# Kernel tuning notes

Hardware: AMD Instinct MI355X
Metric: run time of the kernel (lower is better)

The kernel has to match this reference:

```python
import jax, jax.numpy as jnp
import numpy as np

B, CIN, COUT, K, S, P = 16, 32, 64, 5, 2, 2
D, H, W = 16, 32, 32


def setup_inputs() -> dict:
    key = jax.random.key(0)
    k1, k2, k3 = jax.random.split(key, 3)
    x = jax.random.normal(k1, (B, CIN, D, H, W), dtype=jnp.float32)
    # PyTorch ConvTranspose3d weight layout: (in_channels, out_channels, kD, kH, kW)
    fan = CIN * K * K * K
    bound = 1.0 / np.sqrt(fan)
    weight = jax.random.uniform(k2, (CIN, COUT, K, K, K), dtype=jnp.float32, minval=-bound, maxval=bound)
    bias = jax.random.uniform(k3, (COUT,), dtype=jnp.float32, minval=-bound, maxval=bound)
    return {"x": x, "weight": weight, "bias": bias}


def _maxpool3d(y, k):
    # MaxPool3d with kernel=stride=k, no padding (PyTorch default stride=kernel)
    return jax.lax.reduce_window(y, -jnp.inf, jax.lax.max,
                                 (1, 1, k, k, k), (1, 1, k, k, k), 'VALID')


def reference(x, weight, bias):
    # ConvTranspose3d == conv with lhs_dilation=stride, padding k-1-p, flipped kernel,
    # with (in,out) kernel axes swapped to OIDHW.
    kernel = jnp.flip(weight, axis=(2, 3, 4)).transpose(1, 0, 2, 3, 4)  # (COUT, CIN, K, K, K)
    y = jax.lax.conv_general_dilated(
        x, kernel,
        window_strides=(1, 1, 1),
        padding=[(K - 1 - P, K - 1 - P)] * 3,
        lhs_dilation=(S, S, S),
        dimension_numbers=('NCDHW', 'OIDHW', 'NCDHW'))  # [B, COUT, 31, 63, 63]
    y = y + bias[None, :, None, None, None]
    y = _maxpool3d(y, 2)   # [B, COUT, 15, 31, 31]
    y = _maxpool3d(y, 3)   # [B, COUT, 5, 10, 10]
    return jnp.sum(y, axis=1, keepdims=True)  # [B, 1, 5, 10, 10]
```

## Files before the change

kernel.cpp:

```cpp
#include <hip/hip_runtime.h>


typedef __attribute__((ext_vector_type(8))) short short8;
typedef __attribute__((ext_vector_type(4))) float f32x4;

#define CIN 32
#define COUT 64

static __device__ __forceinline__ short f2bf(float f) {
  unsigned u = __float_as_uint(f);
  return (short)((u + 0x7fffu + ((u >> 16) & 1u)) >> 16);
}

__global__ __launch_bounds__(256) void reorder_w(const float* __restrict__ w,
                                                 short* __restrict__ wr) {
  const int t = blockIdx.x * 256 + threadIdx.x;
  const int l = t & 63, mt = (t >> 6) & 3, tap = t >> 8;
  const int cout = 16 * mt + (l & 15);
  const int kb = l >> 4;
  short8 v;
#pragma unroll
  for (int j = 0; j < 8; ++j)
    v[j] = f2bf(w[((8 * kb + j) * COUT + cout) * 125 + tap]);
  *(short8*)&wr[t * 8] = v;
}

#define E0 (0ULL | 1ULL<<6 | 2ULL<<12 | 27ULL<<18 | 52ULL<<24 | 5ULL<<30 | 6ULL<<36 | 7ULL<<42)
#define E1 (32ULL | 25ULL<<6 | 26ULL<<12 | 51ULL<<18 | 12ULL<<24 | 37ULL<<30 | 30ULL<<36 | 55ULL<<42)
#define O0 (56ULL | 57ULL<<6 | 50ULL<<12 | 11ULL<<18 | 36ULL<<24 | 61ULL<<30 | 62ULL<<36 | 31ULL<<42)
#define O1 (0ULL | 1ULL<<6 | 10ULL<<12 | 35ULL<<18 | 60ULL<<24 | 5ULL<<30 | 6ULL<<36 | 7ULL<<42)

__global__ __launch_bounds__(512) void convt_mfma_r11(
    const float* __restrict__ x, const short* __restrict__ wr,
    const float* __restrict__ bias, float* __restrict__ out) {
  __shared__ short xs[8 * 4 * 125 * 8];
  __shared__ float red[16];

  const int orig = blockIdx.x;
  const int bi = (orig & 7) * 125 + (orig >> 3);
  const int bg = bi / 500, r = bi % 500;
  const int od = r / 100, oh = (r / 10) % 10, ow = r % 10;
  const int tid = threadIdx.x;
  const int d0 = 3 * od - 1, h0 = 3 * oh - 1, w0 = 3 * ow - 1;
  const int xoff0 = d0 * 1024 + h0 * 32 + w0;

  for (int e = tid; e < 8 * 4 * 128; e += 512) {
    const int pos = e & 127;
    if (pos < 125) {
      const int kb = (e >> 7) & 3, bb = e >> 9;
      const int id = pos / 25, rem = pos - 25 * id;
      const int ih = rem / 5, iw = rem - 5 * ih;
      const bool ok = (d0 + id) >= 0 && (h0 + ih) >= 0 && (w0 + iw) >= 0;
      const float* xp =
          x + ((size_t)((bg * 8 + bb) * CIN + kb * 8) << 14) + xoff0 + id * 1024 + ih * 32 + iw;
      short8 v8;
#pragma unroll
      for (int j = 0; j < 8; ++j) v8[j] = f2bf(ok ? xp[j << 14] : 0.f);
      *(short8*)&xs[(bb * 500 + kb * 125 + pos) * 8] = v8;
    }
  }
  __syncthreads();

  const int lane = tid & 63, wv = tid >> 6;
  const int mhat = wv >> 2;
  const int bp = wv & 3;
  const int kb = lane >> 4, c = lane & 15;

  const int pos_e = (int)((c < 8 ? (E0 >> (6 * c)) : (E1 >> (6 * (c - 8)))) & 63ULL);
  const int pos_o = (int)((c < 8 ? (O0 >> (6 * c)) : (O1 >> (6 * (c - 8)))) & 63ULL);

  int baddr[4];
#pragma unroll
  for (int i = 0; i < 4; ++i) {
    const int bb = 2 * bp + (i >> 1);
    baddr[i] = (bb * 500 + kb * 125 + ((i & 1) ? pos_o : pos_e)) * 8;
  }

  float mreg[2][2][4];
#pragma unroll
  for (int mm = 0; mm < 2; ++mm)
#pragma unroll
    for (int bl = 0; bl < 2; ++bl)
#pragma unroll
      for (int q = 0; q < 4; ++q) mreg[mm][bl][q] = -__builtin_inff();

  const short* __restrict__ wbase = wr + (2 * mhat) * 512 + lane * 8;

#pragma unroll 1
  for (int p = 0; p < 8; ++p) {
    const int pd = p >> 2, ph = (p >> 1) & 1, pw = p & 1;
    f32x4 acc[2][4];
#pragma unroll
    for (int mm = 0; mm < 2; ++mm)
#pragma unroll
      for (int i = 0; i < 4; ++i) acc[mm][i] = (f32x4){0.f, 0.f, 0.f, 0.f};

#pragma unroll 1
    for (int td = 0; td <= 2 - pd; ++td)
      for (int th = 0; th <= 2 - ph; ++th)
        for (int tw = 0; tw <= 2 - pw; ++tw) {
          const int tap = (pd + 2 * td) * 25 + (ph + 2 * th) * 5 + (pw + 2 * tw);
          const int toff8 = ((2 - td) * 25 + (2 - th) * 5 + (2 - tw)) * 8;
          short8 af[2];
#pragma unroll
          for (int mm = 0; mm < 2; ++mm)
            af[mm] = *(const short8*)(wbase + tap * 2048 + mm * 512);
          short8 bfr[4];
#pragma unroll
          for (int i = 0; i < 4; ++i)
            bfr[i] = *(const short8*)&xs[baddr[i] + toff8];
#pragma unroll
          for (int mm = 0; mm < 2; ++mm)
#pragma unroll
            for (int i = 0; i < 4; ++i)
              acc[mm][i] = __builtin_amdgcn_mfma_f32_16x16x32_bf16(
                  af[mm], bfr[i], acc[mm][i], 0, 0, 0);
        }

#pragma unroll
    for (int mm = 0; mm < 2; ++mm)
#pragma unroll
      for (int bl = 0; bl < 2; ++bl)
#pragma unroll
        for (int q = 0; q < 4; ++q)
          mreg[mm][bl][q] = fmaxf(mreg[mm][bl][q],
                                  fmaxf(acc[mm][2 * bl][q], acc[mm][2 * bl + 1][q]));
  }

#pragma unroll
  for (int bl = 0; bl < 2; ++bl) {
    float s = 0.f;
#pragma unroll
    for (int mm = 0; mm < 2; ++mm)
#pragma unroll
      for (int q = 0; q < 4; ++q) {
        float v = mreg[mm][bl][q];
        v = fmaxf(v, __shfl_xor(v, 1));
        v = fmaxf(v, __shfl_xor(v, 2));
        v = fmaxf(v, __shfl_xor(v, 4));
        v = fmaxf(v, __shfl_xor(v, 8));
        s += v + bias[32 * mhat + 16 * mm + 4 * kb + q];
      }
    s += __shfl_xor(s, 16);
    s += __shfl_xor(s, 32);
    if (lane == 0) red[mhat * 8 + 2 * bp + bl] = s;
  }
  __syncthreads();
  if (tid < 8) {
    out[(bg * 8 + tid) * 500 + r] = red[tid] + red[8 + tid];
  }
}

__global__ __launch_bounds__(256) void fused_convt_pool(
    const float* __restrict__ x, const float* __restrict__ w,
    const float* __restrict__ bias, float* __restrict__ out) {
  __shared__ float xsf[CIN * 125];
  __shared__ float ws[COUT * 125];
  __shared__ float red[256];
  const int bi = blockIdx.x;
  const int b = bi / 500;
  const int r = bi % 500;
  const int od = r / 100, oh = (r / 10) % 10, ow = r % 10;
  const int tid = threadIdx.x;
  const int d0 = 3 * od - 1, h0 = 3 * oh - 1, w0 = 3 * ow - 1;
  for (int e = tid; e < CIN * 125; e += 256) {
    const int cin = e / 125, q = e % 125;
    const int id = q / 25, ih = (q / 5) % 5, iw = q % 5;
    const int gd = d0 + id, gh = h0 + ih, gw = w0 + iw;
    float v = 0.f;
    if (gd >= 0 && gh >= 0 && gw >= 0)
      v = x[(((b * CIN + cin) * 16 + gd) * 32 + gh) * 32 + gw];
    xsf[e] = v;
  }
  const int cout = tid >> 2;
  const int vs = tid & 3;
  int cellbase[7];
#pragma unroll
  for (int j = 0; j < 7; ++j) {
    int cell = vs + 4 * j;
    if (cell > 26) cell = 26;
    cellbase[j] = (cell / 9) * 25 + ((cell / 3) % 3) * 5 + cell % 3;
  }
  float acc[7][8];
#pragma unroll
  for (int j = 0; j < 7; ++j)
#pragma unroll
    for (int p = 0; p < 8; ++p) acc[j][p] = 0.f;
  for (int cin = 0; cin < CIN; ++cin) {
    __syncthreads();
    const float* wg = w + cin * (COUT * 125);
    for (int e = tid; e < COUT * 125; e += 256) ws[e] = wg[e];
    __syncthreads();
    const float* xc = xsf + cin * 125;
    const float* wc = ws + cout * 125;
#pragma unroll
    for (int pd = 0; pd < 2; ++pd)
#pragma unroll
      for (int ph = 0; ph < 2; ++ph)
#pragma unroll
        for (int pw = 0; pw < 2; ++pw) {
          const int P = pd * 4 + ph * 2 + pw;
          for (int td = 0; td <= 2 - pd; ++td)
            for (int th = 0; th <= 2 - ph; ++th)
              for (int tw = 0; tw <= 2 - pw; ++tw) {
                const float wv2 =
                    wc[(pd + 2 * td) * 25 + (ph + 2 * th) * 5 + (pw + 2 * tw)];
                const float* xp = xc + (2 - td) * 25 + (2 - th) * 5 + (2 - tw);
#pragma unroll
                for (int j = 0; j < 7; ++j)
                  acc[j][P] = fmaf(wv2, xp[cellbase[j]], acc[j][P]);
              }
        }
  }
  float m = acc[0][0];
#pragma unroll
  for (int j = 0; j < 7; ++j)
#pragma unroll
    for (int p = 0; p < 8; ++p) m = fmaxf(m, acc[j][p]);
  red[tid] = m;
  __syncthreads();
  if (tid < 64) {
    float cm = fmaxf(fmaxf(red[tid * 4 + 0], red[tid * 4 + 1]),
                     fmaxf(red[tid * 4 + 2], red[tid * 4 + 3]));
    cm += bias[tid];
    for (int off = 32; off > 0; off >>= 1) cm += __shfl_down(cm, off);
    if (tid == 0) out[bi] = cm;
  }
}

extern "C" void kernel_launch(void* const* d_in, const int* in_sizes, int n_in,
                              void* d_out, int out_size, void* d_ws, size_t ws_size,
                              hipStream_t stream) {
  const float* x = (const float*)d_in[0];
  const float* wgt = (const float*)d_in[1];
  const float* bias = (const float*)d_in[2];
  float* out = (float*)d_out;
  const size_t wr_bytes = 125 * 4 * 64 * 8 * sizeof(short);
  if (ws_size >= wr_bytes) {
    short* wr = (short*)d_ws;
    reorder_w<<<125, 256, 0, stream>>>(wgt, wr);
    convt_mfma_r11<<<1000, 512, 0, stream>>>(x, wr, bias, out);
  } else {
    fused_convt_pool<<<8000, 256, 0, stream>>>(x, wgt, bias, out);
  }
}
```

Before: 136.0 us.

## Halve batch group per block and reuse B fragments across depth taps

Each block now handles 4 batches instead of 8, using 256 threads and 2000 blocks, which halves shared memory per block so more blocks can be resident. The tap loop is restructured so both depth parities are accumulated together: for each (h,w) tap, the three depth-shifted B fragments are loaded once from LDS and reused across five depth-tap MFMA groups. This cuts LDS reads per MFMA. In exchange it doubles the accumulator registers and uses more fragment registers, which may lower occupancy. The x tile is now loaded and converted for 2000 blocks instead of 1000, but each tile covers half as many batches.

```diff
diff --git a/kernel.cpp b/kernel.cpp
--- a/kernel.cpp
+++ b/kernel.cpp
@@ -30,21 +30,21 @@
 #define O0 (56ULL | 57ULL<<6 | 50ULL<<12 | 11ULL<<18 | 36ULL<<24 | 61ULL<<30 | 62ULL<<36 | 31ULL<<42)
 #define O1 (0ULL | 1ULL<<6 | 10ULL<<12 | 35ULL<<18 | 60ULL<<24 | 5ULL<<30 | 6ULL<<36 | 7ULL<<42)
 
-__global__ __launch_bounds__(512) void convt_mfma_r11(
+__global__ __launch_bounds__(256) void convt_mfma_r14(
     const float* __restrict__ x, const short* __restrict__ wr,
     const float* __restrict__ bias, float* __restrict__ out) {
-  __shared__ short xs[8 * 4 * 125 * 8];
-  __shared__ float red[16];
+  __shared__ short xs[4 * 4 * 125 * 8];
+  __shared__ float red[8];
 
   const int orig = blockIdx.x;
-  const int bi = (orig & 7) * 125 + (orig >> 3);
+  const int bi = (orig & 7) * 250 + (orig >> 3);
   const int bg = bi / 500, r = bi % 500;
   const int od = r / 100, oh = (r / 10) % 10, ow = r % 10;
   const int tid = threadIdx.x;
   const int d0 = 3 * od - 1, h0 = 3 * oh - 1, w0 = 3 * ow - 1;
   const int xoff0 = d0 * 1024 + h0 * 32 + w0;
 
-  for (int e = tid; e < 8 * 4 * 128; e += 512) {
+  for (int e = tid; e < 4 * 4 * 128; e += 256) {
     const int pos = e & 127;
     if (pos < 125) {
       const int kb = (e >> 7) & 3, bb = e >> 9;
@@ -52,7 +52,7 @@
       const int ih = rem / 5, iw = rem - 5 * ih;
       const bool ok = (d0 + id) >= 0 && (h0 + ih) >= 0 && (w0 + iw) >= 0;
       const float* xp =
-          x + ((size_t)((bg * 8 + bb) * CIN + kb * 8) << 14) + xoff0 + id * 1024 + ih * 32 + iw;
+          x + ((size_t)((bg * 4 + bb) * CIN + kb * 8) << 14) + xoff0 + id * 1024 + ih * 32 + iw;
       short8 v8;
 #pragma unroll
       for (int j = 0; j < 8; ++j) v8[j] = f2bf(ok ? xp[j << 14] : 0.f);
@@ -62,8 +62,8 @@
   __syncthreads();
 
   const int lane = tid & 63, wv = tid >> 6;
-  const int mhat = wv >> 2;
-  const int bp = wv & 3;
+  const int mhat = wv >> 1;
+  const int bp = wv & 1;
   const int kb = lane >> 4, c = lane & 15;
 
   const int pos_e = (int)((c < 8 ? (E0 >> (6 * c)) : (E1 >> (6 * (c - 8)))) & 63ULL);
@@ -86,46 +86,62 @@
 
   const short* __restrict__ wbase = wr + (2 * mhat) * 512 + lane * 8;
 
+#define DTAP(PD, TD)                                                              \
+  {                                                                               \
+    const short8 a0v = *(const short8*)(wt + (PD + 2 * TD) * 25 * 2048);          \
+    const short8 a1v = *(const short8*)(wt + (PD + 2 * TD) * 25 * 2048 + 512);    \
+    _Pragma("unroll") for (int i = 0; i < 4; ++i) {                               \
+      acc[PD][0][i] = __builtin_amdgcn_mfma_f32_16x16x32_bf16(                    \
+          a0v, B3[2 - TD][i], acc[PD][0][i], 0, 0, 0);                            \
+      acc[PD][1][i] = __builtin_amdgcn_mfma_f32_16x16x32_bf16(                    \
+          a1v, B3[2 - TD][i], acc[PD][1][i], 0, 0, 0);                            \
+    }                                                                             \
+  }
+
 #pragma unroll 1
-  for (int p = 0; p < 8; ++p) {
-    const int pd = p >> 2, ph = (p >> 1) & 1, pw = p & 1;
-    f32x4 acc[2][4];
-#pragma unroll
-    for (int mm = 0; mm < 2; ++mm)
-#pragma unroll
-      for (int i = 0; i < 4; ++i) acc[mm][i] = (f32x4){0.f, 0.f, 0.f, 0.f};
+  for (int php = 0; php < 4; ++php) {
+    const int PH = php >> 1, PW = php & 1;
+    f32x4 acc[2][2][4];
+#pragma unroll
+    for (int pd = 0; pd < 2; ++pd)
+#pragma unroll
+      for (int mm = 0; mm < 2; ++mm)
+#pragma unroll
+        for (int i = 0; i < 4; ++i) acc[pd][mm][i] = (f32x4){0.f, 0.f, 0.f, 0.f};
 
 #pragma unroll 1
-    for (int td = 0; td <= 2 - pd; ++td)
-      for (int th = 0; th <= 2 - ph; ++th)
-        for (int tw = 0; tw <= 2 - pw; ++tw) {
-          const int tap = (pd + 2 * td) * 25 + (ph + 2 * th) * 5 + (pw + 2 * tw);
-          const int toff8 = ((2 - td) * 25 + (2 - th) * 5 + (2 - tw)) * 8;
-          short8 af[2];
-#pragma unroll
-          for (int mm = 0; mm < 2; ++mm)
-            af[mm] = *(const short8*)(wbase + tap * 2048 + mm * 512);
-          short8 bfr[4];
+    for (int th = 0; th <= 2 - PH; ++th) {
+#pragma unroll 1
+      for (int tw = 0; tw <= 2 - PW; ++tw) {
+        const int hwoff8 = ((2 - th) * 5 + (2 - tw)) * 8;
+        short8 B3[3][4];
+#pragma unroll
+        for (int dd = 0; dd < 3; ++dd)
 #pragma unroll
           for (int i = 0; i < 4; ++i)
-            bfr[i] = *(const short8*)&xs[baddr[i] + toff8];
-#pragma unroll
-          for (int mm = 0; mm < 2; ++mm)
-#pragma unroll
-            for (int i = 0; i < 4; ++i)
-              acc[mm][i] = __builtin_amdgcn_mfma_f32_16x16x32_bf16(
-                  af[mm], bfr[i], acc[mm][i], 0, 0, 0);
-        }
-
-#pragma unroll
-    for (int mm = 0; mm < 2; ++mm)
-#pragma unroll
-      for (int bl = 0; bl < 2; ++bl)
-#pragma unroll
-        for (int q = 0; q < 4; ++q)
-          mreg[mm][bl][q] = fmaxf(mreg[mm][bl][q],
-                                  fmaxf(acc[mm][2 * bl][q], acc[mm][2 * bl + 1][q]));
-  }
+            B3[dd][i] = *(const short8*)&xs[baddr[i] + hwoff8 + dd * 200];
+
+        const short* wt = wbase + ((PH + 2 * th) * 5 + (PW + 2 * tw)) * 2048;
+        DTAP(0, 0)
+        DTAP(0, 1)
+        DTAP(0, 2)
+        DTAP(1, 0)
+        DTAP(1, 1)
+      }
+    }
+
+#pragma unroll
+    for (int pd = 0; pd < 2; ++pd)
+#pragma unroll
+      for (int mm = 0; mm < 2; ++mm)
+#pragma unroll
+        for (int bl = 0; bl < 2; ++bl)
+#pragma unroll
+          for (int q = 0; q < 4; ++q)
+            mreg[mm][bl][q] = fmaxf(mreg[mm][bl][q],
+                                    fmaxf(acc[pd][mm][2 * bl][q], acc[pd][mm][2 * bl + 1][q]));
+  }
+#undef DTAP
 
 #pragma unroll
   for (int bl = 0; bl < 2; ++bl) {
@@ -143,11 +159,11 @@
       }
     s += __shfl_xor(s, 16);
     s += __shfl_xor(s, 32);
-    if (lane == 0) red[mhat * 8 + 2 * bp + bl] = s;
+    if (lane == 0) red[mhat * 4 + 2 * bp + bl] = s;
   }
   __syncthreads();
-  if (tid < 8) {
-    out[(bg * 8 + tid) * 500 + r] = red[tid] + red[8 + tid];
+  if (tid < 4) {
+    out[(bg * 4 + tid) * 500 + r] = red[tid] + red[4 + tid];
   }
 }
 
@@ -239,7 +255,7 @@
   if (ws_size >= wr_bytes) {
     short* wr = (short*)d_ws;
     reorder_w<<<125, 256, 0, stream>>>(wgt, wr);
-    convt_mfma_r11<<<1000, 512, 0, stream>>>(x, wr, bias, out);
+    convt_mfma_r14<<<2000, 256, 0, stream>>>(x, wr, bias, out);
   } else {
     fused_convt_pool<<<8000, 256, 0, stream>>>(x, wgt, bias, out);
   }
```

After: 139.5 us. 1.03x slower.
